# Performance work log

Measured on AMD Instinct MI355X. Metric: run time of the kernel, lower is better.

Reference implementation:

```python
import jax, jax.numpy as jnp
import numpy as np


def get_rel_pos(q_size, k_size, rel_pos):
    # sizes are static python ints; rel_pos has length 2*max(q_size,k_size)-1
    q_ratio = max(k_size / q_size, 1.0)
    k_ratio = max(q_size / k_size, 1.0)
    dist = (np.arange(q_size)[:, None] * q_ratio
            - (np.arange(k_size)[None, :] + (1.0 - k_size)) * k_ratio).astype(np.int64)
    return rel_pos[dist]  # [q_size, k_size, head_dim]


def decomposed_rel_pos_3d(qh, q_thw, k_thw, rel_pos_t, rel_pos_h, rel_pos_w):
    # qh: [B, Q, n_heads, head_dim]
    q_t, q_h, q_w = q_thw
    k_t, k_h, k_w = k_thw
    Rt = get_rel_pos(q_t, k_t, rel_pos_t)
    Rh = get_rel_pos(q_h, k_h, rel_pos_h)
    Rw = get_rel_pos(q_w, k_w, rel_pos_w)
    B = qh.shape[0]
    n, c = qh.shape[2], qh.shape[3]
    q6 = qh.reshape(B, q_t, q_h, q_w, n, c)
    rel_t = jnp.einsum('bthwnc,tkc->bnthwk', q6, Rt)
    rel_h = jnp.einsum('bthwnc,hkc->bnthwk', q6, Rh)
    rel_w = jnp.einsum('bthwnc,wkc->bnthwk', q6, Rw)
    bias = (rel_t[:, :, :, :, :, :, None, None]
            + rel_h[:, :, :, :, :, None, :, None]
            + rel_w[:, :, :, :, :, None, None, :])
    return bias.reshape(B, n, q_t * q_h * q_w, k_t * k_h * k_w)


def setup_inputs() -> dict:
    key = jax.random.key(0)
    ks = jax.random.split(key, 16)
    B, dim, num_heads = 2, 768, 12
    head_dim = dim // num_heads
    q_thw = (8, 14, 14)
    k_thw = (8, 14, 14)
    Q = q_thw[0] * q_thw[1] * q_thw[2]
    K = k_thw[0] * k_thw[1] * k_thw[2]
    s = 0.02
    inp = {
        'q': jax.random.normal(ks[0], (B, Q, dim), jnp.float32),
        'k': jax.random.normal(ks[1], (B, K, dim), jnp.float32),
        'Wq': jax.random.normal(ks[2], (dim, dim), jnp.float32) * s,
        'bq': jnp.zeros((dim,), jnp.float32),
        'Wk': jax.random.normal(ks[3], (dim, dim), jnp.float32) * s,
        'bk': jnp.zeros((dim,), jnp.float32),
        'Wv': jax.random.normal(ks[4], (dim, dim), jnp.float32) * s,
        'bv': jnp.zeros((dim,), jnp.float32),
        'Wo': jax.random.normal(ks[5], (dim, dim), jnp.float32) * s,
        'bo': jnp.zeros((dim,), jnp.float32),
        'rel_pos_t': jax.random.normal(ks[6], (2 * max(q_thw[0], k_thw[0]) - 1, head_dim), jnp.float32) * s,
        'rel_pos_h': jax.random.normal(ks[7], (2 * max(q_thw[1], k_thw[1]) - 1, head_dim), jnp.float32) * s,
        'rel_pos_w': jax.random.normal(ks[8], (2 * max(q_thw[2], k_thw[2]) - 1, head_dim), jnp.float32) * s,
        'q_t': q_thw[0], 'q_h': q_thw[1], 'q_w': q_thw[2],
        'k_t': k_thw[0], 'k_h': k_thw[1], 'k_w': k_thw[2],
    }
    return inp


def reference(q, k, Wq, bq, Wk, bk, Wv, bv, Wo, bo,
              rel_pos_t, rel_pos_h, rel_pos_w,
              q_t, q_h, q_w, k_t, k_h, k_w):
    B, Q, dim = q.shape
    num_heads = 12
    c = dim // num_heads
    scale = 1.0 / np.sqrt(c).astype(np.float32)
    qh = (q @ Wq.T + bq).reshape(B, -1, num_heads, c)   # [B,Q,n,c]
    vh = (k @ Wv.T + bv).reshape(B, -1, num_heads, c)   # [B,K,n,c]
    kh = (k @ Wk.T + bk).reshape(B, -1, num_heads, c)   # [B,K,n,c]
    bias = decomposed_rel_pos_3d(qh, (q_t, q_h, q_w), (k_t, k_h, k_w),
                                 rel_pos_t, rel_pos_h, rel_pos_w)  # [B,n,Q,K]
    scores = jnp.einsum('bqnc,bknc->bnqk', qh, kh) * scale + bias
    attn = jax.nn.softmax(scores, axis=-1)
    out = jnp.einsum('bnqk,bknc->bqnc', attn, vh).reshape(B, Q, dim)
    return out @ Wo.T + bo
```

## Files before the change

kernel.cpp:

```cpp
#include <hip/hip_runtime.h>
#include <math.h>

typedef __bf16 bf16_t;
typedef __bf16 bf16x4 __attribute__((ext_vector_type(4)));
typedef __bf16 bf16x8 __attribute__((ext_vector_type(8)));
typedef float floatx4 __attribute__((ext_vector_type(4)));

#define MFMA16(A, B, C) __builtin_amdgcn_mfma_f32_16x16x32_bf16((A), (B), (C), 0, 0, 0)

static constexpr int BB  = 2;
static constexpr int NH  = 12;
static constexpr int HD  = 64;
static constexpr int DIM = 768;
static constexpr int QS  = 1568;
static constexpr int KS  = 1568;
static constexpr int KSP = 1664;
static constexpr int MROWS = BB * QS;
static constexpr int KT  = 64;

__device__ __forceinline__ void async16(const void* g, void* l) {
    __builtin_amdgcn_global_load_lds(
        (const __attribute__((address_space(1))) unsigned int*)g,
        (__attribute__((address_space(3))) unsigned int*)l, 16, 0, 0);
}

__global__ __launch_bounds__(256) void cvt_w(
    const float* __restrict__ wq, const float* __restrict__ wk,
    const float* __restrict__ wv, const float* __restrict__ wo,
    bf16_t* __restrict__ Wb, bf16_t* __restrict__ vT)
{
    const int NW = DIM * DIM / 4;
    int i = blockIdx.x * 256 + threadIdx.x;
    if (i < 4 * NW) {
        const int w = i / NW;
        const int off = i - w * NW;
        const float* src = (w == 0) ? wq : (w == 1) ? wk : (w == 2) ? wv : wo;
        floatx4 v = ((const floatx4*)src)[off];
        bf16x4 o;
#pragma unroll
        for (int r = 0; r < 4; ++r) o[r] = (bf16_t)v[r];
        ((bf16x4*)(Wb + (size_t)w * DIM * DIM))[off] = o;
        return;
    }
    const int PADC = (KSP - KS) / 8;
    int p = i - 4 * NW;
    if (p < BB * NH * HD * PADC) {
        const int row = p / PADC;
        const int ch  = p - row * PADC;
        bf16x8 z;
#pragma unroll
        for (int r = 0; r < 8; ++r) z[r] = (bf16_t)0.f;
        *(bf16x8*)(vT + (size_t)row * KSP + KS + ch * 8) = z;
    }
}

__global__ __launch_bounds__(256) void gemm_qkv(
    const float* __restrict__ q, const float* __restrict__ k,
    const bf16_t* __restrict__ Wb,
    const float* __restrict__ bq, const float* __restrict__ bk,
    const float* __restrict__ bv,
    bf16_t* __restrict__ qhP, bf16_t* __restrict__ khP, bf16_t* __restrict__ vT)
{
    __shared__ __align__(16) float  Asa[128 * 32];
    __shared__ __align__(16) float  Asb[128 * 32];
    __shared__ __align__(16) bf16_t Bsa[64 * 32];
    __shared__ __align__(16) bf16_t Bsb[64 * 32];

    const int tid   = threadIdx.x;
    const int lane  = tid & 63;
    const int wave  = tid >> 6;
    const int row16 = lane & 15;
    const int quad  = lane >> 4;
    const int wm    = wave & 1;
    const int wn    = wave >> 1;
    const int m0 = blockIdx.x * 128;
    const int yb = blockIdx.y;
    const int proj = yb / 12;
    const int n0 = (yb - proj * 12) * 64;

    const float* X = (proj == 0) ? q : k;
    const bf16_t* W = Wb + (size_t)proj * DIM * DIM;
    const float* bias = (proj == 0) ? bq : (proj == 1) ? bk : bv;

    floatx4 acc[4][2];
#pragma unroll
    for (int mt = 0; mt < 4; ++mt)
#pragma unroll
        for (int nt = 0; nt < 2; ++nt) acc[mt][nt] = (floatx4){0.f, 0.f, 0.f, 0.f};

    auto stage = [&](int k0, float* An, bf16_t* Bn) {
#pragma unroll
        for (int p = 0; p < 4; ++p) {
            const int s = p * 256 + tid;
            const int row = s >> 3, pc = s & 7;
            const int g = pc ^ (row & 7);
            const int rowc = min(m0 + row, MROWS - 1);
            async16(X + (size_t)rowc * DIM + k0 + g * 4, An + s * 4);
        }
        {
            const int row = tid >> 2, pc = tid & 3;
            const int g = pc ^ (row & 3);
            async16(W + (size_t)(n0 + row) * DIM + k0 + g * 8, Bn + tid * 8);
        }
    };

    auto body = [&](int k0, const float* Ac, const bf16_t* Bc,
                    float* An, bf16_t* Bn, bool pf) {
        __syncthreads();
        if (pf) stage(k0 + 32, An, Bn);

        bf16x8 aF[4], bF[2];
#pragma unroll
        for (int mt = 0; mt < 4; ++mt) {
            const int rowA = wm * 64 + mt * 16 + row16;
            const int p0 = (quad * 2) ^ (row16 & 7);
            const int p1 = (quad * 2 + 1) ^ (row16 & 7);
            floatx4 lo = *(const floatx4*)&Ac[rowA * 32 + p0 * 4];
            floatx4 hi = *(const floatx4*)&Ac[rowA * 32 + p1 * 4];
            bf16x8 a;
#pragma unroll
            for (int j = 0; j < 4; ++j) { a[j] = (bf16_t)lo[j]; a[4 + j] = (bf16_t)hi[j]; }
            aF[mt] = a;
        }
#pragma unroll
        for (int nt = 0; nt < 2; ++nt) {
            const int rowB = wn * 32 + nt * 16 + row16;
            const int pb = quad ^ (row16 & 3);
            bF[nt] = *(const bf16x8*)&Bc[rowB * 32 + pb * 8];
        }
#pragma unroll
        for (int mt = 0; mt < 4; ++mt)
#pragma unroll
            for (int nt = 0; nt < 2; ++nt)
                acc[mt][nt] = MFMA16(aF[mt], bF[nt], acc[mt][nt]);
    };

    stage(0, Asa, Bsa);
    for (int ii = 0; ii < 12; ++ii) {
        const int k0 = ii * 64;
        body(k0,      Asa, Bsa, Asb, Bsb, true);
        body(k0 + 32, Asb, Bsb, Asa, Bsa, k0 + 64 < DIM);
    }

#pragma unroll
    for (int nt = 0; nt < 2; ++nt) {
        const int col = n0 + wn * 32 + nt * 16 + row16;
        const int head = col >> 6, cl = col & 63;
        const float bv_ = bias[col];
#pragma unroll
        for (int mt = 0; mt < 4; ++mt) {
            const int row0 = m0 + wm * 64 + mt * 16 + quad * 4;
            if (row0 < MROWS) {
                const int bb = (row0 >= KS) ? 1 : 0;
                const int key0 = row0 - bb * KS;
                if (proj == 2) {
                    bf16x4 pv;
#pragma unroll
                    for (int r = 0; r < 4; ++r) pv[r] = (bf16_t)(acc[mt][nt][r] + bv_);
                    *(bf16x4*)&vT[((size_t)(bb * NH + head) * 64 + cl) * KSP + key0] = pv;
                } else {
                    bf16_t* dst = (proj == 0) ? qhP : khP;
#pragma unroll
                    for (int r = 0; r < 4; ++r)
                        dst[((size_t)(bb * NH + head) * KS + key0 + r) * 64 + cl] =
                            (bf16_t)(acc[mt][nt][r] + bv_);
                }
            }
        }
    }
}

__global__ __launch_bounds__(256, 3) void attn_fused(
    const bf16_t* __restrict__ qhP, const bf16_t* __restrict__ khP,
    const bf16_t* __restrict__ vT,
    const float* __restrict__ rpt, const float* __restrict__ rph,
    const float* __restrict__ rpw, bf16_t* __restrict__ ao)
{
    __shared__ __align__(16) bf16_t KsA[64 * 64];
    __shared__ __align__(16) bf16_t KsB[64 * 64];
    __shared__ __align__(16) bf16_t VsA[64 * 64];
    __shared__ __align__(16) bf16_t VsB[64 * 64];
    __shared__ __align__(16) bf16_t Pl[4 * 16 * 72];
    __shared__ float relS[36 * 64];

    const int tid   = threadIdx.x;
    const int lane  = tid & 63;
    const int wave  = tid >> 6;
    const int row16 = lane & 15;
    const int quad  = lane >> 4;

    const int L = blockIdx.x;
    const int xcd = L & 7;
    const int j = L >> 3;
    const int bn = xcd * 3 + (j % 3);
    const int q0 = (j / 3) * 64;
    const int b = bn / NH;
    const int n = bn - b * NH;

    const float LOG2E = 1.4426950408889634f;
    const float SCALE_L2E = 0.125f * LOG2E;

    for (int i = tid; i < 36 * 64; i += 256) {
        const int e  = i >> 6;
        const int ql = i & 63;
        const int qg = min(q0 + ql, QS - 1);
        const float* tp;
        if (e < 8)       { int tq = qg / 196;       tp = rpt + (size_t)(tq - e + 7) * HD; }
        else if (e < 22) { int hq = (qg / 14) % 14; tp = rph + (size_t)(hq - (e - 8) + 13) * HD; }
        else             { int wq = qg % 14;        tp = rpw + (size_t)(wq - (e - 22) + 13) * HD; }
        const bf16_t* qp = qhP + ((size_t)bn * QS + qg) * 64;
        float s = 0.f;
#pragma unroll
        for (int jj = 0; jj < 8; ++jj) {
            bf16x8 a = *(const bf16x8*)(qp + jj * 8);
            floatx4 t0 = *(const floatx4*)(tp + jj * 8);
            floatx4 t1 = *(const floatx4*)(tp + jj * 8 + 4);
#pragma unroll
            for (int r = 0; r < 4; ++r) s += (float)a[r] * t0[r];
#pragma unroll
            for (int r = 0; r < 4; ++r) s += (float)a[4 + r] * t1[r];
        }
        relS[e * 64 + ql] = s * LOG2E;
    }

    const int qrow = min(q0 + wave * 16 + row16, QS - 1);
    const bf16_t* qp = qhP + ((size_t)bn * QS + qrow) * 64 + quad * 8;
    bf16x8 aQ0 = *(const bf16x8*)(qp);
    bf16x8 aQ1 = *(const bf16x8*)(qp + 32);

    floatx4 O[4];
#pragma unroll
    for (int ct = 0; ct < 4; ++ct) O[ct] = (floatx4){0.f, 0.f, 0.f, 0.f};
    float lsum[4] = {0.f, 0.f, 0.f, 0.f};

    const bf16_t* khb = khP + (size_t)bn * KS * 64;
    const bf16_t* vTb = vT + (size_t)bn * 64 * KSP;
    const int rowb  = wave * 16 + quad * 4;
    const int pbase = (wave * 16) * 72;

    auto stageKV = [&](int k0, bf16_t* Kn, bf16_t* Vn) {
#pragma unroll
        for (int p = 0; p < 2; ++p) {
            const int s = p * 256 + tid;
            const int row = s >> 3, c = s & 7;
            const int g = c ^ (row & 7);
            async16(khb + (size_t)min(k0 + row, KS - 1) * 64 + g * 8, Kn + s * 8);
            async16(vTb + (size_t)row * KSP + k0 + g * 8, Vn + s * 8);
        }
    };

    auto iter = [&](int ki, const bf16_t* Kc, const bf16_t* Vc,
                    bf16_t* Kn, bf16_t* Vn, bool pf) {
        const int k0 = ki * KT;
        __syncthreads();
        if (pf) stageKV(k0 + KT, Kn, Vn);

        floatx4 S[4];
#pragma unroll
        for (int t = 0; t < 4; ++t) {
            const int row = t * 16 + row16;
            const int rsw = row & 7;
            const bf16_t* kp_ = &Kc[row * 64];
            floatx4 s = (floatx4){0.f, 0.f, 0.f, 0.f};
            s = MFMA16(aQ0, *(const bf16x8*)&kp_[(quad ^ rsw) * 8], s);
            s = MFMA16(aQ1, *(const bf16x8*)&kp_[((quad + 4) ^ rsw) * 8], s);
            S[t] = s;
        }

#pragma unroll
        for (int t = 0; t < 4; ++t) {
            const int key = k0 + t * 16 + row16;
            const int kt = key / 196;
            const int rem = key - kt * 196;
            const int kho = rem / 14;
            const int kwo = rem - kho * 14;
            floatx4 bias = *(const floatx4*)&relS[kt * 64 + rowb];
            bias = bias + *(const floatx4*)&relS[(8 + kho) * 64 + rowb];
            bias = bias + *(const floatx4*)&relS[(22 + kwo) * 64 + rowb];
            const bool ok = (key < KS);
#pragma unroll
            for (int r = 0; r < 4; ++r) {
                float p = __builtin_amdgcn_exp2f(S[t][r] * SCALE_L2E + bias[r]);
                p = ok ? p : 0.f;
                lsum[r] += p;
                Pl[pbase + (quad * 4 + r) * 72 + t * 16 + row16] = (bf16_t)p;
            }
        }

        bf16x8 aP[2];
#pragma unroll
        for (int c4 = 0; c4 < 2; ++c4)
            aP[c4] = *(const bf16x8*)&Pl[pbase + row16 * 72 + c4 * 32 + quad * 8];
#pragma unroll
        for (int ct = 0; ct < 4; ++ct) {
            const int row = ct * 16 + row16;
            const int rsw = row & 7;
            const bf16_t* vp_ = &Vc[row * 64];
            floatx4 o = O[ct];
            o = MFMA16(aP[0], *(const bf16x8*)&vp_[(quad ^ rsw) * 8], o);
            o = MFMA16(aP[1], *(const bf16x8*)&vp_[((quad + 4) ^ rsw) * 8], o);
            O[ct] = o;
        }
    };

    stageKV(0, KsA, VsA);
#pragma unroll 1
    for (int kp2 = 0; kp2 < 12; ++kp2) {
        iter(2 * kp2,     KsA, VsA, KsB, VsB, true);
        iter(2 * kp2 + 1, KsB, VsB, KsA, VsA, true);
    }
    iter(24, KsA, VsA, KsB, VsB, false);

    float inv[4];
#pragma unroll
    for (int r = 0; r < 4; ++r) {
        float l = lsum[r];
        l += __shfl_xor(l, 1);
        l += __shfl_xor(l, 2);
        l += __shfl_xor(l, 4);
        l += __shfl_xor(l, 8);
        inv[r] = 1.f / l;
    }
#pragma unroll
    for (int ct = 0; ct < 4; ++ct) {
        const int c = n * HD + ct * 16 + row16;
#pragma unroll
        for (int r = 0; r < 4; ++r) {
            const int qr = q0 + wave * 16 + quad * 4 + r;
            if (qr < QS)
                ao[(size_t)(b * QS + qr) * DIM + c] = (bf16_t)(O[ct][r] * inv[r]);
        }
    }
}

__global__ __launch_bounds__(256) void gemm_o(
    const bf16_t* __restrict__ X, const bf16_t* __restrict__ W,
    const float* __restrict__ bias, float* __restrict__ Y)
{
    __shared__ __align__(16) bf16_t Asa[64 * 64];
    __shared__ __align__(16) bf16_t Asb[64 * 64];
    __shared__ __align__(16) bf16_t Bsa[64 * 64];
    __shared__ __align__(16) bf16_t Bsb[64 * 64];

    const int tid   = threadIdx.x;
    const int lane  = tid & 63;
    const int wave  = tid >> 6;
    const int row16 = lane & 15;
    const int quad  = lane >> 4;
    const int m0 = blockIdx.x * 64;
    const int n0 = blockIdx.y * 64;

    floatx4 acc[4];
#pragma unroll
    for (int nt = 0; nt < 4; ++nt) acc[nt] = (floatx4){0.f, 0.f, 0.f, 0.f};

    auto stage = [&](int k0, bf16_t* An, bf16_t* Bn) {
#pragma unroll
        for (int p = 0; p < 2; ++p) {
            const int s = p * 256 + tid;
            const int row = s >> 3, pc = s & 7;
            const int g = pc ^ (row & 7);
            async16(X + (size_t)(m0 + row) * DIM + k0 + g * 8, An + s * 8);
            async16(W + (size_t)(n0 + row) * DIM + k0 + g * 8, Bn + s * 8);
        }
    };

    auto body = [&](int k0, const bf16_t* Ac, const bf16_t* Bc,
                    bf16_t* An, bf16_t* Bn, bool pf) {
        __syncthreads();
        if (pf) stage(k0 + 64, An, Bn);
#pragma unroll
        for (int h = 0; h < 2; ++h) {
            const int lc = h * 4 + quad;
            const int pa = lc ^ (row16 & 7);
            const int rowA = wave * 16 + row16;
            bf16x8 aF = *(const bf16x8*)&Ac[rowA * 64 + pa * 8];
#pragma unroll
            for (int nt = 0; nt < 4; ++nt) {
                bf16x8 bF = *(const bf16x8*)&Bc[(nt * 16 + row16) * 64 + pa * 8];
                acc[nt] = MFMA16(aF, bF, acc[nt]);
            }
        }
    };

    stage(0, Asa, Bsa);
    for (int ii = 0; ii < 6; ++ii) {
        const int k0 = ii * 128;
        body(k0,      Asa, Bsa, Asb, Bsb, true);
        body(k0 + 64, Asb, Bsb, Asa, Bsa, k0 + 128 < DIM);
    }

#pragma unroll
    for (int nt = 0; nt < 4; ++nt) {
        const int col = n0 + nt * 16 + row16;
        const float bv = bias[col];
#pragma unroll
        for (int r = 0; r < 4; ++r) {
            const int row = m0 + wave * 16 + quad * 4 + r;
            Y[(size_t)row * DIM + col] = acc[nt][r] + bv;
        }
    }
}

extern "C" void kernel_launch(void* const* d_in, const int* in_sizes, int n_in,
                              void* d_out, int out_size, void* d_ws, size_t ws_size,
                              hipStream_t stream) {
    const float* q   = (const float*)d_in[0];
    const float* k   = (const float*)d_in[1];
    const float* Wq  = (const float*)d_in[2];
    const float* bq  = (const float*)d_in[3];
    const float* Wk  = (const float*)d_in[4];
    const float* bk  = (const float*)d_in[5];
    const float* Wv  = (const float*)d_in[6];
    const float* bv  = (const float*)d_in[7];
    const float* Wo  = (const float*)d_in[8];
    const float* bo  = (const float*)d_in[9];
    const float* rpt = (const float*)d_in[10];
    const float* rph = (const float*)d_in[11];
    const float* rpw = (const float*)d_in[12];

    bf16_t* qhP = (bf16_t*)d_ws;
    bf16_t* khP = qhP + (size_t)MROWS * DIM;
    bf16_t* vT  = khP + (size_t)MROWS * DIM;
    bf16_t* ao  = vT  + (size_t)BB * NH * HD * KSP;
    bf16_t* Wb  = ao  + (size_t)MROWS * DIM;

    const int NCVT = 4 * (DIM * DIM / 4) + BB * NH * HD * ((KSP - KS) / 8);
    cvt_w<<<(NCVT + 255) / 256, 256, 0, stream>>>(Wq, Wk, Wv, Wo, Wb, vT);

    gemm_qkv<<<dim3(25, 36), 256, 0, stream>>>(q, k, Wb, bq, bk, bv, qhP, khP, vT);

    attn_fused<<<dim3(8 * 3 * 25), 256, 0, stream>>>(
        qhP, khP, vT, rpt, rph, rpw, ao);

    gemm_o<<<dim3(MROWS / 64, DIM / 64), 256, 0, stream>>>(
        ao, Wb + (size_t)3 * DIM * DIM, bo, (float*)d_out);
}
```

Measured before the change: 240.9 us.

## Fold relative-position bias into QK MFMA via extended Q and one-hot K

A new qext kernel computes each query's 36 rel-pos dot products once per query, pre-scaled by log2(e), into an extended bf16 Q tensor. cvt_w now writes a one-hot key tensor that marks each key's t/h/w index, and the K projection is pre-scaled by scale·log2(e). The attention kernel therefore gets the full biased logit from a 128-deep MFMA, replacing the per-element relS lookups, adds and scaling. The key tile shrinks from 64 to 32, with occupancy hint 2 instead of 3, so it divides KS exactly and drops the tail masking and vT padding. This trades roughly double QK MFMA work, an extra kernel launch and a bf16-rounded bias for less VALU and LDS work in the softmax loop.

```diff
diff --git a/kernel.cpp b/kernel.cpp
--- a/kernel.cpp
+++ b/kernel.cpp
@@ -16,7 +16,10 @@
 static constexpr int KS  = 1568;
 static constexpr int KSP = 1664;
 static constexpr int MROWS = BB * QS;
-static constexpr int KT  = 64;
+static constexpr int KT  = 32;
+
+static constexpr float LOG2E = 1.4426950408889634f;
+static constexpr float SCALE_L2E = 0.125f * LOG2E;
 
 __device__ __forceinline__ void async16(const void* g, void* l) {
     __builtin_amdgcn_global_load_lds(
@@ -27,7 +30,7 @@
 __global__ __launch_bounds__(256) void cvt_w(
     const float* __restrict__ wq, const float* __restrict__ wk,
     const float* __restrict__ wv, const float* __restrict__ wo,
-    bf16_t* __restrict__ Wb, bf16_t* __restrict__ vT)
+    bf16_t* __restrict__ Wb, bf16_t* __restrict__ koh)
 {
     const int NW = DIM * DIM / 4;
     int i = blockIdx.x * 256 + threadIdx.x;
@@ -42,15 +45,23 @@
         ((bf16x4*)(Wb + (size_t)w * DIM * DIM))[off] = o;
         return;
     }
-    const int PADC = (KSP - KS) / 8;
-    int p = i - 4 * NW;
-    if (p < BB * NH * HD * PADC) {
-        const int row = p / PADC;
-        const int ch  = p - row * PADC;
-        bf16x8 z;
-#pragma unroll
-        for (int r = 0; r < 8; ++r) z[r] = (bf16_t)0.f;
-        *(bf16x8*)(vT + (size_t)row * KSP + KS + ch * 8) = z;
+    const int key = i - 4 * NW;
+    if (key < KS) {
+        const int tk = key / 196;
+        const int rem = key - tk * 196;
+        const int hk = rem / 14;
+        const int wk_ = rem - hk * 14;
+#pragma unroll
+        for (int c8 = 0; c8 < 8; ++c8) {
+            bf16x8 v;
+#pragma unroll
+            for (int j = 0; j < 8; ++j) {
+                const int e = c8 * 8 + j;
+                const float f = (e == tk || e == 8 + hk || e == 22 + wk_) ? 1.f : 0.f;
+                v[j] = (bf16_t)f;
+            }
+            *(bf16x8*)(koh + (size_t)key * 64 + c8 * 8) = v;
+        }
     }
 }
 
@@ -81,6 +92,7 @@
     const float* X = (proj == 0) ? q : k;
     const bf16_t* W = Wb + (size_t)proj * DIM * DIM;
     const float* bias = (proj == 0) ? bq : (proj == 1) ? bk : bv;
+    const float osc = (proj == 1) ? SCALE_L2E : 1.0f;
 
     floatx4 acc[4][2];
 #pragma unroll
@@ -163,25 +175,61 @@
 #pragma unroll
                     for (int r = 0; r < 4; ++r)
                         dst[((size_t)(bb * NH + head) * KS + key0 + r) * 64 + cl] =
-                            (bf16_t)(acc[mt][nt][r] + bv_);
+                            (bf16_t)((acc[mt][nt][r] + bv_) * osc);
                 }
             }
         }
     }
 }
 
-__global__ __launch_bounds__(256, 3) void attn_fused(
-    const bf16_t* __restrict__ qhP, const bf16_t* __restrict__ khP,
-    const bf16_t* __restrict__ vT,
+__global__ __launch_bounds__(256) void qext(
+    const bf16_t* __restrict__ qhP,
     const float* __restrict__ rpt, const float* __restrict__ rph,
-    const float* __restrict__ rpw, bf16_t* __restrict__ ao)
+    const float* __restrict__ rpw, bf16_t* __restrict__ Qe)
 {
-    __shared__ __align__(16) bf16_t KsA[64 * 64];
-    __shared__ __align__(16) bf16_t KsB[64 * 64];
-    __shared__ __align__(16) bf16_t VsA[64 * 64];
-    __shared__ __align__(16) bf16_t VsB[64 * 64];
-    __shared__ __align__(16) bf16_t Pl[4 * 16 * 72];
-    __shared__ float relS[36 * 64];
+    const int tid = threadIdx.x;
+    const int row = blockIdx.x * 4 + (tid >> 6);
+    const int e   = tid & 63;
+    const int bn  = row / QS;
+    const int qg  = row - bn * QS;
+    const int tq  = qg / 196;
+    const int rem = qg - tq * 196;
+    const int hq  = rem / 14;
+    const int wq  = rem - hq * 14;
+
+    float val = 0.f;
+    if (e < 36) {
+        const float* tp;
+        if (e < 8)       tp = rpt + (size_t)(tq - e + 7) * HD;
+        else if (e < 22) tp = rph + (size_t)(hq - (e - 8) + 13) * HD;
+        else             tp = rpw + (size_t)(wq - (e - 22) + 13) * HD;
+        const bf16_t* qp = qhP + (size_t)row * 64;
+        float s = 0.f;
+#pragma unroll
+        for (int jj = 0; jj < 8; ++jj) {
+            bf16x8 a = *(const bf16x8*)(qp + jj * 8);
+            floatx4 t0 = *(const floatx4*)(tp + jj * 8);
+            floatx4 t1 = *(const floatx4*)(tp + jj * 8 + 4);
+#pragma unroll
+            for (int r = 0; r < 4; ++r) s += (float)a[r] * t0[r];
+#pragma unroll
+            for (int r = 0; r < 4; ++r) s += (float)a[4 + r] * t1[r];
+        }
+        val = s * LOG2E;
+    }
+    Qe[(size_t)row * 64 + e] = (bf16_t)val;
+}
+
+__global__ __launch_bounds__(256, 2) void attn_fused(
+    const bf16_t* __restrict__ qhP, const bf16_t* __restrict__ Qe,
+    const bf16_t* __restrict__ khP, const bf16_t* __restrict__ koh,
+    const bf16_t* __restrict__ vT, bf16_t* __restrict__ ao)
+{
+    __shared__ __align__(16) bf16_t KsA[32 * 128];
+    __shared__ __align__(16) bf16_t KsB[32 * 128];
+    __shared__ __align__(16) bf16_t VsA[64 * 32];
+    __shared__ __align__(16) bf16_t VsB[64 * 32];
+    __shared__ __align__(16) bf16_t Pl[4 * 16 * 40];
 
     const int tid   = threadIdx.x;
     const int lane  = tid & 63;
@@ -197,36 +245,13 @@
     const int b = bn / NH;
     const int n = bn - b * NH;
 
-    const float LOG2E = 1.4426950408889634f;
-    const float SCALE_L2E = 0.125f * LOG2E;
-
-    for (int i = tid; i < 36 * 64; i += 256) {
-        const int e  = i >> 6;
-        const int ql = i & 63;
-        const int qg = min(q0 + ql, QS - 1);
-        const float* tp;
-        if (e < 8)       { int tq = qg / 196;       tp = rpt + (size_t)(tq - e + 7) * HD; }
-        else if (e < 22) { int hq = (qg / 14) % 14; tp = rph + (size_t)(hq - (e - 8) + 13) * HD; }
-        else             { int wq = qg % 14;        tp = rpw + (size_t)(wq - (e - 22) + 13) * HD; }
-        const bf16_t* qp = qhP + ((size_t)bn * QS + qg) * 64;
-        float s = 0.f;
-#pragma unroll
-        for (int jj = 0; jj < 8; ++jj) {
-            bf16x8 a = *(const bf16x8*)(qp + jj * 8);
-            floatx4 t0 = *(const floatx4*)(tp + jj * 8);
-            floatx4 t1 = *(const floatx4*)(tp + jj * 8 + 4);
-#pragma unroll
-            for (int r = 0; r < 4; ++r) s += (float)a[r] * t0[r];
-#pragma unroll
-            for (int r = 0; r < 4; ++r) s += (float)a[4 + r] * t1[r];
-        }
-        relS[e * 64 + ql] = s * LOG2E;
-    }
-
     const int qrow = min(q0 + wave * 16 + row16, QS - 1);
     const bf16_t* qp = qhP + ((size_t)bn * QS + qrow) * 64 + quad * 8;
+    const bf16_t* qe = Qe  + ((size_t)bn * QS + qrow) * 64 + quad * 8;
     bf16x8 aQ0 = *(const bf16x8*)(qp);
     bf16x8 aQ1 = *(const bf16x8*)(qp + 32);
+    bf16x8 aQ2 = *(const bf16x8*)(qe);
+    bf16x8 aQ3 = *(const bf16x8*)(qe + 32);
 
     floatx4 O[4];
 #pragma unroll
@@ -235,17 +260,25 @@
 
     const bf16_t* khb = khP + (size_t)bn * KS * 64;
     const bf16_t* vTb = vT + (size_t)bn * 64 * KSP;
-    const int rowb  = wave * 16 + quad * 4;
-    const int pbase = (wave * 16) * 72;
+    const int pbase = wave * 16 * 40;
+    const int sw3 = row16 & 7;
+    const int sw2 = (row16 >> 1) & 3;
 
     auto stageKV = [&](int k0, bf16_t* Kn, bf16_t* Vn) {
 #pragma unroll
         for (int p = 0; p < 2; ++p) {
             const int s = p * 256 + tid;
-            const int row = s >> 3, c = s & 7;
-            const int g = c ^ (row & 7);
-            async16(khb + (size_t)min(k0 + row, KS - 1) * 64 + g * 8, Kn + s * 8);
-            async16(vTb + (size_t)row * KSP + k0 + g * 8, Vn + s * 8);
+            const int row = s >> 4, c = s & 15;
+            const int l = c ^ (row & 7);
+            const bf16_t* src = (l < 8)
+                ? khb + (size_t)(k0 + row) * 64 + l * 8
+                : koh + (size_t)(k0 + row) * 64 + (l - 8) * 8;
+            async16(src, Kn + s * 8);
+        }
+        {
+            const int row = tid >> 2, c = tid & 3;
+            const int l = c ^ ((row >> 1) & 3);
+            async16(vTb + (size_t)row * KSP + k0 + l * 8, Vn + tid * 8);
         }
     };
 
@@ -255,61 +288,43 @@
         __syncthreads();
         if (pf) stageKV(k0 + KT, Kn, Vn);
 
-        floatx4 S[4];
-#pragma unroll
-        for (int t = 0; t < 4; ++t) {
-            const int row = t * 16 + row16;
-            const int rsw = row & 7;
-            const bf16_t* kp_ = &Kc[row * 64];
+        floatx4 S[2];
+#pragma unroll
+        for (int t = 0; t < 2; ++t) {
+            const bf16_t* kp_ = &Kc[(t * 16 + row16) * 128];
             floatx4 s = (floatx4){0.f, 0.f, 0.f, 0.f};
-            s = MFMA16(aQ0, *(const bf16x8*)&kp_[(quad ^ rsw) * 8], s);
-            s = MFMA16(aQ1, *(const bf16x8*)&kp_[((quad + 4) ^ rsw) * 8], s);
+            s = MFMA16(aQ0, *(const bf16x8*)&kp_[((0 + quad) ^ sw3) * 8], s);
+            s = MFMA16(aQ1, *(const bf16x8*)&kp_[((4 + quad) ^ sw3) * 8], s);
+            s = MFMA16(aQ2, *(const bf16x8*)&kp_[((8 + quad) ^ sw3) * 8], s);
+            s = MFMA16(aQ3, *(const bf16x8*)&kp_[((12 + quad) ^ sw3) * 8], s);
             S[t] = s;
         }
 
 #pragma unroll
-        for (int t = 0; t < 4; ++t) {
-            const int key = k0 + t * 16 + row16;
-            const int kt = key / 196;
-            const int rem = key - kt * 196;
-            const int kho = rem / 14;
-            const int kwo = rem - kho * 14;
-            floatx4 bias = *(const floatx4*)&relS[kt * 64 + rowb];
-            bias = bias + *(const floatx4*)&relS[(8 + kho) * 64 + rowb];
-            bias = bias + *(const floatx4*)&relS[(22 + kwo) * 64 + rowb];
-            const bool ok = (key < KS);
+        for (int t = 0; t < 2; ++t) {
 #pragma unroll
             for (int r = 0; r < 4; ++r) {
-                float p = __builtin_amdgcn_exp2f(S[t][r] * SCALE_L2E + bias[r]);
-                p = ok ? p : 0.f;
+                float p = __builtin_amdgcn_exp2f(S[t][r]);
                 lsum[r] += p;
-                Pl[pbase + (quad * 4 + r) * 72 + t * 16 + row16] = (bf16_t)p;
+                Pl[pbase + (quad * 4 + r) * 40 + t * 16 + row16] = (bf16_t)p;
             }
         }
 
-        bf16x8 aP[2];
-#pragma unroll
-        for (int c4 = 0; c4 < 2; ++c4)
-            aP[c4] = *(const bf16x8*)&Pl[pbase + row16 * 72 + c4 * 32 + quad * 8];
+        bf16x8 aP = *(const bf16x8*)&Pl[pbase + row16 * 40 + quad * 8];
 #pragma unroll
         for (int ct = 0; ct < 4; ++ct) {
-            const int row = ct * 16 + row16;
-            const int rsw = row & 7;
-            const bf16_t* vp_ = &Vc[row * 64];
-            floatx4 o = O[ct];
-            o = MFMA16(aP[0], *(const bf16x8*)&vp_[(quad ^ rsw) * 8], o);
-            o = MFMA16(aP[1], *(const bf16x8*)&vp_[((quad + 4) ^ rsw) * 8], o);
-            O[ct] = o;
+            bf16x8 bV = *(const bf16x8*)&Vc[(ct * 16 + row16) * 32 + (quad ^ sw2) * 8];
+            O[ct] = MFMA16(aP, bV, O[ct]);
         }
     };
 
     stageKV(0, KsA, VsA);
 #pragma unroll 1
-    for (int kp2 = 0; kp2 < 12; ++kp2) {
+    for (int kp2 = 0; kp2 < 24; ++kp2) {
         iter(2 * kp2,     KsA, VsA, KsB, VsB, true);
         iter(2 * kp2 + 1, KsB, VsB, KsA, VsA, true);
     }
-    iter(24, KsA, VsA, KsB, VsB, false);
+    iter(48, KsA, VsA, KsB, VsB, false);
 
     float inv[4];
 #pragma unroll
@@ -422,16 +437,20 @@
     bf16_t* qhP = (bf16_t*)d_ws;
     bf16_t* khP = qhP + (size_t)MROWS * DIM;
     bf16_t* vT  = khP + (size_t)MROWS * DIM;
-    bf16_t* ao  = vT  + (size_t)BB * NH * HD * KSP;
+    bf16_t* Qe  = vT  + (size_t)BB * NH * HD * KSP;
+    bf16_t* koh = Qe  + (size_t)MROWS * DIM;
+    bf16_t* ao  = koh + (size_t)KS * 64;
     bf16_t* Wb  = ao  + (size_t)MROWS * DIM;
 
-    const int NCVT = 4 * (DIM * DIM / 4) + BB * NH * HD * ((KSP - KS) / 8);
-    cvt_w<<<(NCVT + 255) / 256, 256, 0, stream>>>(Wq, Wk, Wv, Wo, Wb, vT);
+    const int NCVT = 4 * (DIM * DIM / 4) + KS;
+    cvt_w<<<(NCVT + 255) / 256, 256, 0, stream>>>(Wq, Wk, Wv, Wo, Wb, koh);
 
     gemm_qkv<<<dim3(25, 36), 256, 0, stream>>>(q, k, Wb, bq, bk, bv, qhP, khP, vT);
 
+    qext<<<(BB * NH * QS) / 4, 256, 0, stream>>>(qhP, rpt, rph, rpw, Qe);
+
     attn_fused<<<dim3(8 * 3 * 25), 256, 0, stream>>>(
-        qhP, khP, vT, rpt, rph, rpw, ao);
+        qhP, Qe, khP, koh, vT, ao);
 
     gemm_o<<<dim3(MROWS / 64, DIM / 64), 256, 0, stream>>>(
         ao, Wb + (size_t)3 * DIM * DIM, bo, (float*)d_out);
```

Measured after the change: 257.6 us. 1.07x slower.
